# Kernel optimization log

Hardware: AMD Instinct MI355X
Metric: run time of the kernel (lower is better)

Reference implementation:

```python
import jax, jax.numpy as jnp
import numpy as np

HEAD_SIZE = 128
N_EMBD = 64
B, T = 8, 4096


def setup_inputs() -> dict:
    key = jax.random.key(0)
    k1, k2, k3, k4 = jax.random.split(key, 4)
    x = jax.random.normal(k1, (B, T, N_EMBD), dtype=jnp.float32)
    Wq = jax.random.normal(k2, (N_EMBD, HEAD_SIZE), dtype=jnp.float32) * (N_EMBD ** -0.5)
    Wk = jax.random.normal(k3, (N_EMBD, HEAD_SIZE), dtype=jnp.float32) * (N_EMBD ** -0.5)
    Wv = jax.random.normal(k4, (N_EMBD, HEAD_SIZE), dtype=jnp.float32) * (N_EMBD ** -0.5)
    return {"x": x, "Wq": Wq, "Wk": Wk, "Wv": Wv}


def reference(x, Wq, Wk, Wv):
    # x: [B, T, C]; single-head causal self-attention (nanoGPT Head)
    q = x @ Wq  # [B, T, H]
    k = x @ Wk  # [B, T, H]
    v = x @ Wv  # [B, T, H]
    scale = HEAD_SIZE ** -0.5
    scores = jnp.einsum("bth,bsh->bts", q, k) * scale  # [B, T, T]
    t = x.shape[1]
    causal = jnp.tril(jnp.ones((t, t), dtype=bool))  # [T, T]
    scores = jnp.where(causal[None, :, :], scores, jnp.float32(-jnp.inf))
    wei = jax.nn.softmax(scores, axis=-1)  # [B, T, T]; dropout p=0.0 -> identity
    out = jnp.einsum("bts,bsh->bth", wei, v)  # [B, T, H]
    return out
```

## Files before the change

### kernel.cpp

```cpp
#include <hip/hip_runtime.h>
#include <math.h>

#define BB 8
#define TT 4096
#define CC 64
#define HH 128
#define NTH 256
#define XSTR 72
#define WSTR 72
#define QSCALE ((float)(0.08838834764831845 * 1.4426950408889634))

typedef __attribute__((ext_vector_type(8)))  short short8;
typedef __attribute__((ext_vector_type(4)))  float floatx4;
typedef __attribute__((ext_vector_type(16))) float floatx16;

__device__ __forceinline__ unsigned short f2bf(float f) {
    union { float f; unsigned int u; } un; un.f = f;
    unsigned int r = un.u + 0x7FFF + ((un.u >> 16) & 1);
    return (unsigned short)(r >> 16);
}
__device__ __forceinline__ unsigned int pack2bf_fast(float a, float b) {
    union { float f; unsigned int u; } ua, ub; ua.f = a; ub.f = b;
    return __builtin_amdgcn_perm(ub.u + 0x8000u, ua.u + 0x8000u, 0x07060302u);
}
__device__ __forceinline__ float bflo(unsigned int u) {
    union { unsigned int u; float f; } x; x.u = u << 16; return x.f;
}
__device__ __forceinline__ float bfhi(unsigned int u) {
    union { unsigned int u; float f; } x; x.u = u & 0xffff0000u; return x.f;
}

__device__ __forceinline__ void gl_lds16(const void* g, void* l) {
    __builtin_amdgcn_global_load_lds(
        (const __attribute__((address_space(1))) unsigned int*)g,
        (__attribute__((address_space(3))) unsigned int*)l, 16, 0, 0);
}

__global__ __launch_bounds__(NTH) void qkv_mfma(
    const float* __restrict__ x,
    const float* __restrict__ Wq, const float* __restrict__ Wk, const float* __restrict__ Wv,
    unsigned short* __restrict__ qb, unsigned short* __restrict__ Kf,
    unsigned short* __restrict__ Vf)
{
    __shared__ __align__(16) unsigned short xs[64 * XSTR];
    __shared__ __align__(16) unsigned short Wts[3 * HH * WSTR];

    const int tid  = threadIdx.x;
    const int w    = tid >> 6;
    const int lane = tid & 63;
    const int quad = lane >> 4;
    const int lr   = lane & 15;

    const int b    = blockIdx.x >> 6;
    const int kblk = blockIdx.x & 63;
    const int t0   = kblk * 64;
    const long long rbase = (long long)b * TT + t0;

#pragma unroll
    for (int i = 0; i < 4; ++i) {
        const int idx = tid + i * NTH;
        const int r = idx >> 4, c4 = idx & 15;
        const float4 v = *(const float4*)(x + (rbase + r) * CC + c4 * 4);
        unsigned short tmp[4] = { f2bf(v.x), f2bf(v.y), f2bf(v.z), f2bf(v.w) };
        *(unsigned long long*)&xs[r * XSTR + c4 * 4] = *(unsigned long long*)tmp;
    }
#pragma unroll
    for (int mat = 0; mat < 3; ++mat) {
        const float* W = mat == 0 ? Wq : (mat == 1 ? Wk : Wv);
        const float s = mat == 0 ? QSCALE : 1.0f;
#pragma unroll
        for (int i = 0; i < 32; ++i) {
            const int idx = tid + i * NTH;
            const int c = idx >> 7, h = idx & 127;
            Wts[(mat * HH + h) * WSTR + c] = f2bf(W[idx] * s);
        }
    }
    __syncthreads();

    const short8 bx0 = *(const short8*)&xs[(w * 16 + lr) * XSTR + quad * 8];
    const short8 bx1 = *(const short8*)&xs[(w * 16 + lr) * XSTR + 32 + quad * 8];

    {
        const unsigned short* Wrow = Wts;
#pragma unroll
        for (int ht = 0; ht < 8; ++ht) {
            const short8 aw0 = *(const short8*)(Wrow + (ht * 16 + lr) * WSTR + quad * 8);
            const short8 aw1 = *(const short8*)(Wrow + (ht * 16 + lr) * WSTR + 32 + quad * 8);
            floatx4 acc = (floatx4)0.f;
            acc = __builtin_amdgcn_mfma_f32_16x16x32_bf16(aw0, bx0, acc, 0, 0, 0);
            acc = __builtin_amdgcn_mfma_f32_16x16x32_bf16(aw1, bx1, acc, 0, 0, 0);
            ushort4 st = { f2bf(acc[0]), f2bf(acc[1]), f2bf(acc[2]), f2bf(acc[3]) };
            *(ushort4*)(qb + (rbase + w * 16 + lr) * HH + ht * 16 + quad * 4) = st;
        }
    }
    {
        const unsigned short* Wrow = Wts + 1 * HH * WSTR;
        const int khp = w >> 1;
        const int lqp = (w & 1) * 16 + lr;
        unsigned short* kdst = Kf + ((long long)((b * 64 + kblk) * 2 + khp)) * 4096
                             + ((quad >> 1) & 1) * 256 + lqp * 8 + (quad & 1) * 4;
#pragma unroll
        for (int ht = 0; ht < 8; ++ht) {
            const short8 aw0 = *(const short8*)(Wrow + (ht * 16 + lr) * WSTR + quad * 8);
            const short8 aw1 = *(const short8*)(Wrow + (ht * 16 + lr) * WSTR + 32 + quad * 8);
            floatx4 acc = (floatx4)0.f;
            acc = __builtin_amdgcn_mfma_f32_16x16x32_bf16(aw0, bx0, acc, 0, 0, 0);
            acc = __builtin_amdgcn_mfma_f32_16x16x32_bf16(aw1, bx1, acc, 0, 0, 0);
            ushort4 st = { f2bf(acc[0]), f2bf(acc[1]), f2bf(acc[2]), f2bf(acc[3]) };
            *(ushort4*)(kdst + ht * 512) = st;
        }
    }
    {
        const unsigned short* Wrow = Wts + 2 * HH * WSTR;
        const int khv = w >> 1, ksv = w & 1, lsv = (quad >> 1) & 1;
        unsigned short* vdst = Vf + (long long)(b * 64 + kblk) * 8192 + khv * 4096
                             + ksv * 512 + lsv * 256 + (quad & 1) * 4;
#pragma unroll
        for (int htp = 0; htp < 8; ++htp) {
            const short8 bw0 = *(const short8*)(Wrow + (htp * 16 + lr) * WSTR + quad * 8);
            const short8 bw1 = *(const short8*)(Wrow + (htp * 16 + lr) * WSTR + 32 + quad * 8);
            floatx4 acc = (floatx4)0.f;
            acc = __builtin_amdgcn_mfma_f32_16x16x32_bf16(bx0, bw0, acc, 0, 0, 0);
            acc = __builtin_amdgcn_mfma_f32_16x16x32_bf16(bx1, bw1, acc, 0, 0, 0);
            ushort4 st = { f2bf(acc[0]), f2bf(acc[1]), f2bf(acc[2]), f2bf(acc[3]) };
            *(ushort4*)(vdst + (htp >> 1) * 1024 + ((htp & 1) * 16 + lr) * 8) = st;
        }
    }
}

__device__ __forceinline__ void dma_tile32(
    const unsigned char* __restrict__ Kj, const unsigned char* __restrict__ Vj,
    unsigned char* buf, int w, int lane)
{
    const unsigned char* src;
    unsigned char* dst;
    if (w < 2) { src = Kj + w * 4096 + lane * 16;        dst = buf + w * 4096; }
    else       { src = Vj + (w - 2) * 4096 + lane * 16;  dst = buf + 8192 + (w - 2) * 4096; }
#pragma unroll
    for (int i = 0; i < 4; ++i)
        gl_lds16(src + i * 1024, dst + i * 1024);
}

__global__ __launch_bounds__(NTH, 3) void flash_splitk(
    const unsigned short* __restrict__ qb,
    const unsigned short* __restrict__ Kf,
    const unsigned short* __restrict__ Vf,
    unsigned short* __restrict__ Ob, float* __restrict__ Lb)
{
    __shared__ __align__(16) unsigned char KV[2][16384];

    const int tid  = threadIdx.x;
    const int w    = tid >> 6;
    const int lane = tid & 63;
    const int lq   = lane & 31;
    const int ls   = lane >> 5;

    const int id = blockIdx.x;
    const int b  = id & 7;
    const int c  = (id >> 3) & 3;
    const int qt = 31 - (id >> 5);
    const int len = qt + 1;
    const int lo  = c * len;
    const int hi  = lo + qt;

    const int q0 = qt * 128;
    const long long baset = (long long)b * TT;
    const unsigned char* Kbase = (const unsigned char*)Kf + (long long)b * 128 * 8192;
    const unsigned char* Vbase = (const unsigned char*)Vf + (long long)b * 128 * 8192;

    dma_tile32(Kbase + (long long)lo * 8192, Vbase + (long long)lo * 8192, KV[0], w, lane);

    short8 aq[8];
    {
        const unsigned short* qrp = qb + (baset + q0 + w * 32 + lq) * HH + ls * 8;
#pragma unroll
        for (int st = 0; st < 8; ++st)
            aq[st] = *(const short8*)(qrp + st * 16);
    }

    floatx16 o_acc[4];
#pragma unroll
    for (int ht = 0; ht < 4; ++ht) o_acc[ht] = (floatx16)0.f;
    float l_lane = 0.f;

    for (int j = lo; j <= hi; ++j) {
        const int cb = (j - lo) & 1;
        __syncthreads();
        if (j < hi)
            dma_tile32(Kbase + (long long)(j + 1) * 8192, Vbase + (long long)(j + 1) * 8192,
                       KV[cb ^ 1], w, lane);

        const int D = q0 + w * 32 - j * 32;
        if (D > -32) {
            const unsigned short* Kt = (const unsigned short*)&KV[cb][0];
            const unsigned short* Vt = (const unsigned short*)&KV[cb][8192];

            short8 kfr[8], vfr[8];
#pragma unroll
            for (int st = 0; st < 8; ++st)
                kfr[st] = *(const short8*)(Kt + st * 512 + lane * 8);
#pragma unroll
            for (int i = 0; i < 8; ++i)
                vfr[i] = *(const short8*)(Vt + (i >> 1) * 1024 + (i & 1) * 512 + lane * 8);

            floatx16 s_acc = (floatx16)0.f;
#pragma unroll
            for (int st = 0; st < 8; ++st)
                s_acc = __builtin_amdgcn_mfma_f32_32x32x16_bf16(kfr[st], aq[st], s_acc, 0, 0, 0);

            float p[16];
            if (D < 31) {
#pragma unroll
                for (int reg = 0; reg < 16; ++reg) {
                    const int kk = (reg & 3) + 8 * (reg >> 2) + 4 * ls;
                    p[reg] = (kk <= lq + D) ? __builtin_amdgcn_exp2f(s_acc[reg]) : 0.f;
                }
            } else {
#pragma unroll
                for (int reg = 0; reg < 16; ++reg)
                    p[reg] = __builtin_amdgcn_exp2f(s_acc[reg]);
            }
#pragma unroll
            for (int reg = 0; reg < 16; ++reg) l_lane += p[reg];

            unsigned int g[8], pg[8];
#pragma unroll
            for (int i = 0; i < 8; ++i) g[i] = pack2bf_fast(p[2 * i], p[2 * i + 1]);
#pragma unroll
            for (int i = 0; i < 8; ++i) pg[i] = __shfl_xor((int)g[i], 32);
            short8 bp[2];
#pragma unroll
            for (int ks = 0; ks < 2; ++ks) {
                union { short8 s; unsigned int u[4]; } fr;
                const int bs = ks * 4;
                if (ls == 0) {
                    fr.u[0] = g[bs];      fr.u[1] = g[bs + 1];
                    fr.u[2] = pg[bs];     fr.u[3] = pg[bs + 1];
                } else {
                    fr.u[0] = pg[bs + 2]; fr.u[1] = pg[bs + 3];
                    fr.u[2] = g[bs + 2];  fr.u[3] = g[bs + 3];
                }
                bp[ks] = fr.s;
            }

#pragma unroll
            for (int ht = 0; ht < 4; ++ht) {
                o_acc[ht] = __builtin_amdgcn_mfma_f32_32x32x16_bf16(vfr[ht * 2 + 0], bp[0], o_acc[ht], 0, 0, 0);
                o_acc[ht] = __builtin_amdgcn_mfma_f32_32x32x16_bf16(vfr[ht * 2 + 1], bp[1], o_acc[ht], 0, 0, 0);
            }
        }
    }

    const int pid = ((b * 32 + qt) << 2) + c;
    const float l2 = l_lane + __shfl_xor(l_lane, 32);
    if (lane < 32) Lb[pid * 128 + w * 32 + lq] = l2;

    unsigned short* od = Ob + (long long)pid * 16384 + (w * 32 + lq) * HH;
#pragma unroll
    for (int ht = 0; ht < 4; ++ht)
#pragma unroll
        for (int rg = 0; rg < 4; ++rg) {
            uint2 st;
            st.x = pack2bf_fast(o_acc[ht][rg * 4 + 0], o_acc[ht][rg * 4 + 1]);
            st.y = pack2bf_fast(o_acc[ht][rg * 4 + 2], o_acc[ht][rg * 4 + 3]);
            *(uint2*)(od + ht * 32 + rg * 8 + 4 * ls) = st;
        }
}

__global__ __launch_bounds__(NTH) void combine(
    const unsigned short* __restrict__ Ob, const float* __restrict__ Lb,
    float* __restrict__ out)
{
    const int id = blockIdx.x;
    const int b = id & 7;
    const int rest = id >> 3;
    const int qt = rest >> 1, half = rest & 1;
    const int tid = threadIdx.x;
    const int q = half * 64 + (tid >> 2);
    const int hg = tid & 3;
    const int pid0 = ((b * 32 + qt) << 2);

    float acc[32];
#pragma unroll
    for (int i = 0; i < 32; ++i) acc[i] = 0.f;
    float ltot = 0.f;

#pragma unroll
    for (int c = 0; c < 4; ++c) {
        ltot += Lb[(pid0 + c) * 128 + q];
        const uint4* src = (const uint4*)(Ob + (long long)(pid0 + c) * 16384 + q * HH + hg * 32);
#pragma unroll
        for (int g = 0; g < 4; ++g) {
            const uint4 d = src[g];
            acc[g * 8 + 0] += bflo(d.x); acc[g * 8 + 1] += bfhi(d.x);
            acc[g * 8 + 2] += bflo(d.y); acc[g * 8 + 3] += bfhi(d.y);
            acc[g * 8 + 4] += bflo(d.z); acc[g * 8 + 5] += bfhi(d.z);
            acc[g * 8 + 6] += bflo(d.w); acc[g * 8 + 7] += bfhi(d.w);
        }
    }
    const float inv = 1.f / ltot;
    float* op = out + ((long long)b * TT + qt * 128 + q) * HH + hg * 32;
#pragma unroll
    for (int g = 0; g < 8; ++g) {
        float4 st = make_float4(acc[g * 4 + 0] * inv, acc[g * 4 + 1] * inv,
                                acc[g * 4 + 2] * inv, acc[g * 4 + 3] * inv);
        *(float4*)(op + g * 4) = st;
    }
}

extern "C" void kernel_launch(void* const* d_in, const int* in_sizes, int n_in,
                              void* d_out, int out_size, void* d_ws, size_t ws_size,
                              hipStream_t stream)
{
    const float* x  = (const float*)d_in[0];
    const float* Wq = (const float*)d_in[1];
    const float* Wk = (const float*)d_in[2];
    const float* Wv = (const float*)d_in[3];
    float* out = (float*)d_out;

    const long long n = (long long)BB * TT * HH;
    unsigned short* qb = (unsigned short*)d_ws;
    unsigned short* Kf = qb + n;
    unsigned short* Vf = Kf + n;
    unsigned short* Ob = Vf + n;
    float*          Lb = (float*)(Ob + (long long)1024 * 16384);

    qkv_mfma<<<BB * (TT / 64), NTH, 0, stream>>>(x, Wq, Wk, Wv, qb, Kf, Vf);
    flash_splitk<<<1024, NTH, 0, stream>>>(qb, Kf, Vf, Ob, Lb);
    combine<<<BB * 64, NTH, 0, stream>>>(Ob, Lb, out);
}
```

Measured before the change: 144.0 us.

## Split KV into fixed 8-tile chunks, use permlane32 swap and MFMA priority

Replaces the four-way split of each query tile's KV range with fixed chunks of eight 32-key tiles. Each query tile now gets a variable number of chunks, giving 272 blocks per batch, and the combine kernel loops over a variable chunk count. This evens out per-block work and removes the tail imbalance of the causal triangle. It also swaps the shfl_xor-based P fragment exchange for permlane32_swap, and raises wave priority around the MFMA blocks. In exchange there are more partial outputs to write and reduce, and combine now runs a non-unrolled loop.

```diff
diff --git a/kernel.cpp b/kernel.cpp
--- a/kernel.cpp
+++ b/kernel.cpp
@@ -8,6 +8,7 @@
 #define NTH 256
 #define XSTR 72
 #define WSTR 72
+#define NCH 272
 #define QSCALE ((float)(0.08838834764831845 * 1.4426950408889634))
 
 typedef __attribute__((ext_vector_type(8)))  short short8;
@@ -157,11 +158,17 @@
 
     const int id = blockIdx.x;
     const int b  = id & 7;
-    const int c  = (id >> 3) & 3;
-    const int qt = 31 - (id >> 5);
-    const int len = qt + 1;
-    const int lo  = c * len;
-    const int hi  = lo + qt;
+    const int cc = id >> 3;
+    int p = 0, base = 0;
+    while (cc >= base + (32 - 2 * p)) { base += 32 - 2 * p; ++p; }
+    const int within = cc - base;
+    const int nchp  = 16 - p;
+    const int qt = (within < nchp) ? (31 - 2 * p) : (30 - 2 * p);
+    const int ch = (within < nchp) ? within : within - nchp;
+    const int ntile = 4 * qt + 4;
+    const int lo  = ch * 8;
+    const int len = min(8, ntile - lo);
+    const int hi  = lo + len - 1;
 
     const int q0 = qt * 128;
     const long long baset = (long long)b * TT;
@@ -204,54 +211,60 @@
                 vfr[i] = *(const short8*)(Vt + (i >> 1) * 1024 + (i & 1) * 512 + lane * 8);
 
             floatx16 s_acc = (floatx16)0.f;
+            __builtin_amdgcn_s_setprio(1);
 #pragma unroll
             for (int st = 0; st < 8; ++st)
                 s_acc = __builtin_amdgcn_mfma_f32_32x32x16_bf16(kfr[st], aq[st], s_acc, 0, 0, 0);
-
-            float p[16];
+            __builtin_amdgcn_s_setprio(0);
+
+            float pr[16];
             if (D < 31) {
 #pragma unroll
                 for (int reg = 0; reg < 16; ++reg) {
                     const int kk = (reg & 3) + 8 * (reg >> 2) + 4 * ls;
-                    p[reg] = (kk <= lq + D) ? __builtin_amdgcn_exp2f(s_acc[reg]) : 0.f;
+                    pr[reg] = (kk <= lq + D) ? __builtin_amdgcn_exp2f(s_acc[reg]) : 0.f;
                 }
             } else {
 #pragma unroll
                 for (int reg = 0; reg < 16; ++reg)
-                    p[reg] = __builtin_amdgcn_exp2f(s_acc[reg]);
+                    pr[reg] = __builtin_amdgcn_exp2f(s_acc[reg]);
             }
-#pragma unroll
-            for (int reg = 0; reg < 16; ++reg) l_lane += p[reg];
-
-            unsigned int g[8], pg[8];
-#pragma unroll
-            for (int i = 0; i < 8; ++i) g[i] = pack2bf_fast(p[2 * i], p[2 * i + 1]);
-#pragma unroll
-            for (int i = 0; i < 8; ++i) pg[i] = __shfl_xor((int)g[i], 32);
+            {
+                float s0 = (pr[0] + pr[1]) + (pr[2] + pr[3]);
+                float s1 = (pr[4] + pr[5]) + (pr[6] + pr[7]);
+                float s2 = (pr[8] + pr[9]) + (pr[10] + pr[11]);
+                float s3 = (pr[12] + pr[13]) + (pr[14] + pr[15]);
+                l_lane += (s0 + s1) + (s2 + s3);
+            }
+
+            unsigned int g[8];
+#pragma unroll
+            for (int i = 0; i < 8; ++i) g[i] = pack2bf_fast(pr[2 * i], pr[2 * i + 1]);
             short8 bp[2];
 #pragma unroll
             for (int ks = 0; ks < 2; ++ks) {
+                const int bs = ks * 4;
                 union { short8 s; unsigned int u[4]; } fr;
-                const int bs = ks * 4;
-                if (ls == 0) {
-                    fr.u[0] = g[bs];      fr.u[1] = g[bs + 1];
-                    fr.u[2] = pg[bs];     fr.u[3] = pg[bs + 1];
-                } else {
-                    fr.u[0] = pg[bs + 2]; fr.u[1] = pg[bs + 3];
-                    fr.u[2] = g[bs + 2];  fr.u[3] = g[bs + 3];
-                }
+                auto r0 = __builtin_amdgcn_permlane32_swap((int)g[bs + 0], (int)g[bs + 2], false, false);
+                auto r1 = __builtin_amdgcn_permlane32_swap((int)g[bs + 1], (int)g[bs + 3], false, false);
+                fr.u[0] = (unsigned int)r0[0];
+                fr.u[1] = (unsigned int)r1[0];
+                fr.u[2] = (unsigned int)r0[1];
+                fr.u[3] = (unsigned int)r1[1];
                 bp[ks] = fr.s;
             }
 
+            __builtin_amdgcn_s_setprio(1);
 #pragma unroll
             for (int ht = 0; ht < 4; ++ht) {
                 o_acc[ht] = __builtin_amdgcn_mfma_f32_32x32x16_bf16(vfr[ht * 2 + 0], bp[0], o_acc[ht], 0, 0, 0);
                 o_acc[ht] = __builtin_amdgcn_mfma_f32_32x32x16_bf16(vfr[ht * 2 + 1], bp[1], o_acc[ht], 0, 0, 0);
             }
-        }
-    }
-
-    const int pid = ((b * 32 + qt) << 2) + c;
+            __builtin_amdgcn_s_setprio(0);
+        }
+    }
+
+    const int pid = b * NCH + cc;
     const float l2 = l_lane + __shfl_xor(l_lane, 32);
     if (lane < 32) Lb[pid * 128 + w * 32 + lq] = l2;
 
@@ -278,15 +291,18 @@
     const int tid = threadIdx.x;
     const int q = half * 64 + (tid >> 2);
     const int hg = tid & 3;
-    const int pid0 = ((b * 32 + qt) << 2);
+
+    const int p = (31 - qt) >> 1;
+    const int off = p * (33 - p) + (((31 - qt) & 1) ? (16 - p) : 0);
+    const int count = 16 - p;
+    const int pid0 = b * NCH + off;
 
     float acc[32];
 #pragma unroll
     for (int i = 0; i < 32; ++i) acc[i] = 0.f;
     float ltot = 0.f;
 
-#pragma unroll
-    for (int c = 0; c < 4; ++c) {
+    for (int c = 0; c < count; ++c) {
         ltot += Lb[(pid0 + c) * 128 + q];
         const uint4* src = (const uint4*)(Ob + (long long)(pid0 + c) * 16384 + q * HH + hg * 32);
 #pragma unroll
@@ -323,9 +339,9 @@
     unsigned short* Kf = qb + n;
     unsigned short* Vf = Kf + n;
     unsigned short* Ob = Vf + n;
-    float*          Lb = (float*)(Ob + (long long)1024 * 16384);
+    float*          Lb = (float*)(Ob + (long long)(BB * NCH) * 16384);
 
     qkv_mfma<<<BB * (TT / 64), NTH, 0, stream>>>(x, Wq, Wk, Wv, qb, Kf, Vf);
-    flash_splitk<<<1024, NTH, 0, stream>>>(qb, Kf, Vf, Ob, Lb);
+    flash_splitk<<<BB * NCH, NTH, 0, stream>>>(qb, Kf, Vf, Ob, Lb);
     combine<<<BB * 64, NTH, 0, stream>>>(Ob, Lb, out);
 }
```

After: 191.4 us. 33.0% more time.

## Precompute bf16 weights once and drop LDS staging in flash attention loop

Applied to the files above, without the earlier changes.

Adds a small kernel that converts and transposes Wq/Wk/Wv to bf16 once, so each qkv block copies the prepared weights into LDS with direct global-to-LDS loads instead of converting them itself. The flash kernel no longer double-buffers K/V tiles through shared memory; each wave reads its fragments straight from global/L2, has no __syncthreads, and stops at its own causal bound rather than idling through masked tiles. The occupancy hint rises from 3 to 4 blocks per CU. The trade-off is an extra kernel launch, and K/V reuse across the four waves now depends on the cache rather than shared memory, which may raise global load traffic and latency.

```diff
diff --git a/kernel.cpp b/kernel.cpp
--- a/kernel.cpp
+++ b/kernel.cpp
@@ -36,9 +36,21 @@
         (__attribute__((address_space(3))) unsigned int*)l, 16, 0, 0);
 }
 
+__global__ __launch_bounds__(NTH) void wconv(
+    const float* __restrict__ Wq, const float* __restrict__ Wk, const float* __restrict__ Wv,
+    unsigned short* __restrict__ Wbf)
+{
+    const int id = blockIdx.x * NTH + threadIdx.x;
+    const int mat = id >> 13;
+    const int rem = id & 8191;
+    const int h = rem & 127, c = rem >> 7;
+    const float* W = mat == 0 ? Wq : (mat == 1 ? Wk : Wv);
+    const float s = mat == 0 ? QSCALE : 1.0f;
+    Wbf[(mat * HH + h) * WSTR + c] = f2bf(W[c * HH + h] * s);
+}
+
 __global__ __launch_bounds__(NTH) void qkv_mfma(
-    const float* __restrict__ x,
-    const float* __restrict__ Wq, const float* __restrict__ Wk, const float* __restrict__ Wv,
+    const float* __restrict__ x, const unsigned short* __restrict__ Wbf,
     unsigned short* __restrict__ qb, unsigned short* __restrict__ Kf,
     unsigned short* __restrict__ Vf)
 {
@@ -56,6 +68,16 @@
     const int t0   = kblk * 64;
     const long long rbase = (long long)b * TT + t0;
 
+    {
+        const unsigned char* ws = (const unsigned char*)Wbf;
+        unsigned char* wd = (unsigned char*)Wts;
+#pragma unroll
+        for (int it = 0; it < 14; ++it) {
+            const int off = it * 4096 + tid * 16;
+            if (off < 3 * HH * WSTR * 2)
+                gl_lds16(ws + off, wd + off);
+        }
+    }
 #pragma unroll
     for (int i = 0; i < 4; ++i) {
         const int idx = tid + i * NTH;
@@ -63,17 +85,6 @@
         const float4 v = *(const float4*)(x + (rbase + r) * CC + c4 * 4);
         unsigned short tmp[4] = { f2bf(v.x), f2bf(v.y), f2bf(v.z), f2bf(v.w) };
         *(unsigned long long*)&xs[r * XSTR + c4 * 4] = *(unsigned long long*)tmp;
-    }
-#pragma unroll
-    for (int mat = 0; mat < 3; ++mat) {
-        const float* W = mat == 0 ? Wq : (mat == 1 ? Wk : Wv);
-        const float s = mat == 0 ? QSCALE : 1.0f;
-#pragma unroll
-        for (int i = 0; i < 32; ++i) {
-            const int idx = tid + i * NTH;
-            const int c = idx >> 7, h = idx & 127;
-            Wts[(mat * HH + h) * WSTR + c] = f2bf(W[idx] * s);
-        }
     }
     __syncthreads();
 
@@ -128,27 +139,12 @@
     }
 }
 
-__device__ __forceinline__ void dma_tile32(
-    const unsigned char* __restrict__ Kj, const unsigned char* __restrict__ Vj,
-    unsigned char* buf, int w, int lane)
-{
-    const unsigned char* src;
-    unsigned char* dst;
-    if (w < 2) { src = Kj + w * 4096 + lane * 16;        dst = buf + w * 4096; }
-    else       { src = Vj + (w - 2) * 4096 + lane * 16;  dst = buf + 8192 + (w - 2) * 4096; }
-#pragma unroll
-    for (int i = 0; i < 4; ++i)
-        gl_lds16(src + i * 1024, dst + i * 1024);
-}
-
-__global__ __launch_bounds__(NTH, 3) void flash_splitk(
+__global__ __launch_bounds__(NTH, 4) void flash_splitk(
     const unsigned short* __restrict__ qb,
     const unsigned short* __restrict__ Kf,
     const unsigned short* __restrict__ Vf,
     unsigned short* __restrict__ Ob, float* __restrict__ Lb)
 {
-    __shared__ __align__(16) unsigned char KV[2][16384];
-
     const int tid  = threadIdx.x;
     const int w    = tid >> 6;
     const int lane = tid & 63;
@@ -162,13 +158,12 @@
     const int len = qt + 1;
     const int lo  = c * len;
     const int hi  = lo + qt;
+    const int hiw = min(hi, 4 * qt + w);
 
     const int q0 = qt * 128;
     const long long baset = (long long)b * TT;
-    const unsigned char* Kbase = (const unsigned char*)Kf + (long long)b * 128 * 8192;
-    const unsigned char* Vbase = (const unsigned char*)Vf + (long long)b * 128 * 8192;
-
-    dma_tile32(Kbase + (long long)lo * 8192, Vbase + (long long)lo * 8192, KV[0], w, lane);
+    const unsigned short* Kb = Kf + (long long)b * 128 * 4096;
+    const unsigned short* Vb = Vf + (long long)b * 128 * 4096;
 
     short8 aq[8];
     {
@@ -183,71 +178,63 @@
     for (int ht = 0; ht < 4; ++ht) o_acc[ht] = (floatx16)0.f;
     float l_lane = 0.f;
 
-    for (int j = lo; j <= hi; ++j) {
-        const int cb = (j - lo) & 1;
-        __syncthreads();
-        if (j < hi)
-            dma_tile32(Kbase + (long long)(j + 1) * 8192, Vbase + (long long)(j + 1) * 8192,
-                       KV[cb ^ 1], w, lane);
+    for (int j = lo; j <= hiw; ++j) {
+        const unsigned short* Kt = Kb + (long long)j * 4096;
+        const unsigned short* Vt = Vb + (long long)j * 4096;
+
+        short8 kfr[8], vfr[8];
+#pragma unroll
+        for (int st = 0; st < 8; ++st)
+            kfr[st] = *(const short8*)(Kt + st * 512 + lane * 8);
+#pragma unroll
+        for (int i = 0; i < 8; ++i)
+            vfr[i] = *(const short8*)(Vt + (i >> 1) * 1024 + (i & 1) * 512 + lane * 8);
+
+        floatx16 s_acc = (floatx16)0.f;
+#pragma unroll
+        for (int st = 0; st < 8; ++st)
+            s_acc = __builtin_amdgcn_mfma_f32_32x32x16_bf16(kfr[st], aq[st], s_acc, 0, 0, 0);
 
         const int D = q0 + w * 32 - j * 32;
-        if (D > -32) {
-            const unsigned short* Kt = (const unsigned short*)&KV[cb][0];
-            const unsigned short* Vt = (const unsigned short*)&KV[cb][8192];
-
-            short8 kfr[8], vfr[8];
-#pragma unroll
-            for (int st = 0; st < 8; ++st)
-                kfr[st] = *(const short8*)(Kt + st * 512 + lane * 8);
-#pragma unroll
-            for (int i = 0; i < 8; ++i)
-                vfr[i] = *(const short8*)(Vt + (i >> 1) * 1024 + (i & 1) * 512 + lane * 8);
-
-            floatx16 s_acc = (floatx16)0.f;
-#pragma unroll
-            for (int st = 0; st < 8; ++st)
-                s_acc = __builtin_amdgcn_mfma_f32_32x32x16_bf16(kfr[st], aq[st], s_acc, 0, 0, 0);
-
-            float p[16];
-            if (D < 31) {
-#pragma unroll
-                for (int reg = 0; reg < 16; ++reg) {
-                    const int kk = (reg & 3) + 8 * (reg >> 2) + 4 * ls;
-                    p[reg] = (kk <= lq + D) ? __builtin_amdgcn_exp2f(s_acc[reg]) : 0.f;
-                }
+        float p[16];
+        if (D < 31) {
+#pragma unroll
+            for (int reg = 0; reg < 16; ++reg) {
+                const int kk = (reg & 3) + 8 * (reg >> 2) + 4 * ls;
+                p[reg] = (kk <= lq + D) ? __builtin_amdgcn_exp2f(s_acc[reg]) : 0.f;
+            }
+        } else {
+#pragma unroll
+            for (int reg = 0; reg < 16; ++reg)
+                p[reg] = __builtin_amdgcn_exp2f(s_acc[reg]);
+        }
+#pragma unroll
+        for (int reg = 0; reg < 16; ++reg) l_lane += p[reg];
+
+        unsigned int g[8], pg[8];
+#pragma unroll
+        for (int i = 0; i < 8; ++i) g[i] = pack2bf_fast(p[2 * i], p[2 * i + 1]);
+#pragma unroll
+        for (int i = 0; i < 8; ++i) pg[i] = __shfl_xor((int)g[i], 32);
+        short8 bp[2];
+#pragma unroll
+        for (int ks = 0; ks < 2; ++ks) {
+            union { short8 s; unsigned int u[4]; } fr;
+            const int bs = ks * 4;
+            if (ls == 0) {
+                fr.u[0] = g[bs];      fr.u[1] = g[bs + 1];
+                fr.u[2] = pg[bs];     fr.u[3] = pg[bs + 1];
             } else {
-#pragma unroll
-                for (int reg = 0; reg < 16; ++reg)
-                    p[reg] = __builtin_amdgcn_exp2f(s_acc[reg]);
+                fr.u[0] = pg[bs + 2]; fr.u[1] = pg[bs + 3];
+                fr.u[2] = g[bs + 2];  fr.u[3] = g[bs + 3];
             }
-#pragma unroll
-            for (int reg = 0; reg < 16; ++reg) l_lane += p[reg];
-
-            unsigned int g[8], pg[8];
-#pragma unroll
-            for (int i = 0; i < 8; ++i) g[i] = pack2bf_fast(p[2 * i], p[2 * i + 1]);
-#pragma unroll
-            for (int i = 0; i < 8; ++i) pg[i] = __shfl_xor((int)g[i], 32);
-            short8 bp[2];
-#pragma unroll
-            for (int ks = 0; ks < 2; ++ks) {
-                union { short8 s; unsigned int u[4]; } fr;
-                const int bs = ks * 4;
-                if (ls == 0) {
-                    fr.u[0] = g[bs];      fr.u[1] = g[bs + 1];
-                    fr.u[2] = pg[bs];     fr.u[3] = pg[bs + 1];
-                } else {
-                    fr.u[0] = pg[bs + 2]; fr.u[1] = pg[bs + 3];
-                    fr.u[2] = g[bs + 2];  fr.u[3] = g[bs + 3];
-                }
-                bp[ks] = fr.s;
-            }
-
-#pragma unroll
-            for (int ht = 0; ht < 4; ++ht) {
-                o_acc[ht] = __builtin_amdgcn_mfma_f32_32x32x16_bf16(vfr[ht * 2 + 0], bp[0], o_acc[ht], 0, 0, 0);
-                o_acc[ht] = __builtin_amdgcn_mfma_f32_32x32x16_bf16(vfr[ht * 2 + 1], bp[1], o_acc[ht], 0, 0, 0);
-            }
+            bp[ks] = fr.s;
+        }
+
+#pragma unroll
+        for (int ht = 0; ht < 4; ++ht) {
+            o_acc[ht] = __builtin_amdgcn_mfma_f32_32x32x16_bf16(vfr[ht * 2 + 0], bp[0], o_acc[ht], 0, 0, 0);
+            o_acc[ht] = __builtin_amdgcn_mfma_f32_32x32x16_bf16(vfr[ht * 2 + 1], bp[1], o_acc[ht], 0, 0, 0);
         }
     }
 
@@ -324,8 +311,10 @@
     unsigned short* Vf = Kf + n;
     unsigned short* Ob = Vf + n;
     float*          Lb = (float*)(Ob + (long long)1024 * 16384);
-
-    qkv_mfma<<<BB * (TT / 64), NTH, 0, stream>>>(x, Wq, Wk, Wv, qb, Kf, Vf);
+    unsigned short* Wbf = (unsigned short*)(Lb + 1024 * 128);
+
+    wconv<<<96, NTH, 0, stream>>>(Wq, Wk, Wv, Wbf);
+    qkv_mfma<<<BB * (TT / 64), NTH, 0, stream>>>(x, Wbf, qb, Kf, Vf);
     flash_splitk<<<1024, NTH, 0, stream>>>(qb, Kf, Vf, Ob, Lb);
     combine<<<BB * 64, NTH, 0, stream>>>(Ob, Lb, out);
 }
```

New measurement: 266.1 us. 84.8% more time.
